# Kernel optimization log

Measured on AMD Instinct MI355X. Metric: run time of the kernel, lower is better.

## Reference

```python
import jax, jax.numpy as jnp
import numpy as np

K = 20      # knn fan-in (constructor arg)
EPS = 1e-5  # LayerNorm eps (torch default)

def ln(x, g, b):
    m = jnp.mean(x, axis=-1, keepdims=True)
    v = jnp.mean((x - m) ** 2, axis=-1, keepdims=True)
    return (x - m) / jnp.sqrt(v + EPS) * g + b

def setup_inputs():
    key = jax.random.key(0)
    ks = jax.random.split(key, 12)
    N, Cin, Cout, H = 4096, 128, 128, 512
    def w(k, i, o):
        return (jax.random.normal(k, (i, o), jnp.float32) / np.sqrt(i)).astype(jnp.float32)
    return dict(
        x=jax.random.normal(ks[0], (N, Cin), jnp.float32),
        pos=jax.random.normal(ks[1], (N, 3), jnp.float32),
        batch=jnp.zeros((N,), jnp.int32),
        # PointTransformerConv linears (bias=False in PyG)
        W_lin=w(ks[2], Cin, Cout),
        W_src=w(ks[3], Cin, Cout),
        W_dst=w(ks[4], Cin, Cout),
        # pos_nn: Lin(3,H) LN ELU Lin(H,Cout) LN ELU
        pw1=w(ks[5], 3, H), pb1=jnp.zeros((H,), jnp.float32),
        pg1=jnp.ones((H,), jnp.float32), pbt1=jnp.zeros((H,), jnp.float32),
        pw2=w(ks[6], H, Cout), pb2=jnp.zeros((Cout,), jnp.float32),
        pg2=jnp.ones((Cout,), jnp.float32), pbt2=jnp.zeros((Cout,), jnp.float32),
        # attn_nn: Lin(Cout,H) LN ELU Lin(H,Cout) LN ELU
        aw1=w(ks[7], Cout, H), ab1=jnp.zeros((H,), jnp.float32),
        ag1=jnp.ones((H,), jnp.float32), abt1=jnp.zeros((H,), jnp.float32),
        aw2=w(ks[8], H, Cout), ab2=jnp.zeros((Cout,), jnp.float32),
        ag2=jnp.ones((Cout,), jnp.float32), abt2=jnp.zeros((Cout,), jnp.float32),
    )

def knn_idx(pos):
    # single-graph knn (batch is constant zero); returns [N, K+1] neighbor idx
    # with self-loop appended (PointTransformerConv add_self_loops=True).
    N = pos.shape[0]
    sq = jnp.sum(pos * pos, axis=1)
    d2 = sq[:, None] + sq[None, :] - 2.0 * (pos @ pos.T)      # [N, N]
    d2 = d2.at[jnp.arange(N), jnp.arange(N)].set(jnp.inf)      # loop=False
    _, nbr = jax.lax.top_k(-d2, K)                             # [N, K]
    return jnp.concatenate([nbr, jnp.arange(N)[:, None]], axis=1)

def reference(x, pos, batch, W_lin, W_src, W_dst,
              pw1, pb1, pg1, pbt1, pw2, pb2, pg2, pbt2,
              aw1, ab1, ag1, abt1, aw2, ab2, ag2, abt2):
    idx = knn_idx(pos)                      # [N, K+1] source node per edge
    v = x @ W_lin                           # message values
    a_src = x @ W_src
    a_dst = x @ W_dst
    rel = pos[:, None, :] - pos[idx]        # pos_i - pos_j, [N, K+1, 3]
    h = jax.nn.elu(ln(rel @ pw1 + pb1, pg1, pbt1))
    delta = jax.nn.elu(ln(h @ pw2 + pb2, pg2, pbt2))           # [N, K+1, C]
    alpha = a_dst[:, None, :] - a_src[idx] + delta
    h2 = jax.nn.elu(ln(alpha @ aw1 + ab1, ag1, abt1))
    alpha = jax.nn.elu(ln(h2 @ aw2 + ab2, ag2, abt2))
    alpha = jax.nn.softmax(alpha, axis=1)   # softmax over neighbors of i
    return jnp.sum(alpha * (v[idx] + delta), axis=1)           # [N, C]
```

## Files before the change

kernel.cpp:

```cpp
#include <hip/hip_runtime.h>
#include <math.h>

#define NN    4096
#define CIN   128
#define CO    128
#define HD    512
#define KK    20
#define EE    21
#define EDGES (NN * EE)
#define LNEPS 1e-5f
#define WSZ   65536

typedef unsigned short u16;
typedef unsigned int   u32;
typedef unsigned long long u64;
typedef __attribute__((ext_vector_type(8))) short bf16x8;
typedef __attribute__((ext_vector_type(4))) float f32x4;

#define MFMA16(a,b,c) __builtin_amdgcn_mfma_f32_16x16x32_bf16(a,b,c,0,0,0)

__device__ __forceinline__ u16 f2b(float x) {
    u32 u = __float_as_uint(x);
    u32 r = u + 0x7fffu + ((u >> 16) & 1u);
    return (u16)(r >> 16);
}
__device__ __forceinline__ float b2f(u16 h) {
    return __uint_as_float(((u32)h) << 16);
}

__global__ __launch_bounds__(256) void k_knn(const float* __restrict__ pos,
                                             int* __restrict__ idxg)
{
    int i = blockIdx.x * 4 + (threadIdx.x >> 6);
    int lane = threadIdx.x & 63;
    float px = pos[3*i], py = pos[3*i+1], pz = pos[3*i+2];
    float bd[KK]; int bi[KK];
#pragma unroll
    for (int s = 0; s < KK; ++s) { bd[s] = INFINITY; bi[s] = 0x7fffffff; }
    for (int j = lane; j < NN; j += 64) {
        float dx = px - pos[3*j], dy = py - pos[3*j+1], dz = pz - pos[3*j+2];
        float d2 = dx*dx + dy*dy + dz*dz;
        if (j != i && d2 < bd[KK-1]) {
            float cd = d2; int ci = j;
#pragma unroll
            for (int s = 0; s < KK; ++s) {
                bool sw = cd < bd[s];
                float td = sw ? bd[s] : cd;  int ti = sw ? bi[s] : ci;
                bd[s] = sw ? cd : bd[s];     bi[s] = sw ? ci : bi[s];
                cd = td; ci = ti;
            }
        }
    }
    for (int r = 0; r < KK; ++r) {
        u64 m = ~0ull;
#pragma unroll
        for (int s = 0; s < KK; ++s) {
            u64 k = ((u64)__float_as_uint(bd[s]) << 32) | (u32)bi[s];
            m = k < m ? k : m;
        }
#pragma unroll
        for (int off = 32; off > 0; off >>= 1) {
            u64 o = __shfl_xor(m, off, 64);
            m = o < m ? o : m;
        }
        if (lane == 0) idxg[i*EE + r] = (int)(u32)m;
#pragma unroll
        for (int s = 0; s < KK; ++s) {
            u64 k = ((u64)__float_as_uint(bd[s]) << 32) | (u32)bi[s];
            if (k == m) bd[s] = INFINITY;
        }
    }
    if (lane == 0) idxg[i*EE + KK] = i;
}

__global__ __launch_bounds__(256) void k_lin3(const float* __restrict__ x,
        const float* __restrict__ Wl, const float* __restrict__ Ws, const float* __restrict__ Wd,
        float* __restrict__ v, float* __restrict__ as_, float* __restrict__ ad)
{
    __shared__ float sx[8][CIN];
    int b = blockIdx.x, t = threadIdx.x;
    int n0 = b * 8;
    for (int q = t; q < 8*CIN; q += 256) sx[q >> 7][q & 127] = x[n0*CIN + q];
    __syncthreads();
    int c = t & 127, g = t >> 7;
    float al[4] = {0,0,0,0}, asr[4] = {0,0,0,0}, adr[4] = {0,0,0,0};
    for (int k = 0; k < CIN; ++k) {
        float wl = Wl[k*CO + c], ws = Ws[k*CO + c], wd = Wd[k*CO + c];
#pragma unroll
        for (int nn2 = 0; nn2 < 4; ++nn2) {
            float xv = sx[g*4 + nn2][k];
            al[nn2]  = fmaf(xv, wl, al[nn2]);
            asr[nn2] = fmaf(xv, ws, asr[nn2]);
            adr[nn2] = fmaf(xv, wd, adr[nn2]);
        }
    }
#pragma unroll
    for (int nn2 = 0; nn2 < 4; ++nn2) {
        int n = n0 + g*4 + nn2;
        v[n*CO + c]   = al[nn2];
        as_[n*CO + c] = asr[nn2];
        ad[n*CO + c]  = adr[nn2];
    }
}

__global__ __launch_bounds__(256) void k_wconv3(
        const float* __restrict__ aw1, const float* __restrict__ aw2,
        const float* __restrict__ pw2,
        u16* __restrict__ awp1, u16* __restrict__ awp2, u16* __restrict__ pwp2)
{
    int gb = blockIdx.x;
    const float* src; u16* dst; int N, kplog, base; bool split;
    if (gb < 256)      { src = aw1; dst = awp1; N = HD; kplog = 2; base = 0;   split = false; }
    else if (gb < 512) { src = aw2; dst = awp2; N = CO; kplog = 4; base = 256; split = true;  }
    else               { src = pw2; dst = pwp2; N = CO; kplog = 4; base = 512; split = true;  }
    int idx = (gb - base)*256 + threadIdx.x;
    int j  = idx & 7;
    int l  = (idx >> 3) & 63;
    int ks = (idx >> 9) & ((1 << kplog) - 1);
    int nt = idx >> (9 + kplog);
    int k = ks*32 + (l >> 4)*8 + j;
    int c = nt*16 + (l & 15);
    float w = src[(size_t)k*N + c];
    u16 hi = f2b(w);
    dst[idx] = hi;
    if (split) dst[idx + WSZ] = f2b(w - b2f(hi));
}

template<int L, int NW>
__device__ __forceinline__ void ln_elu_b16(u16* base, int rows, int stride,
        const float* __restrict__ gam, const float* __restrict__ bet)
{
    constexpr int P = L / 64;
    int t = threadIdx.x, lane = t & 63, w = t >> 6;
    float g[P], b[P];
#pragma unroll
    for (int q = 0; q < P; q += 4) {
        *(float4*)&g[q] = *(const float4*)&gam[lane*P + q];
        *(float4*)&b[q] = *(const float4*)&bet[lane*P + q];
    }
    for (int e = w; e < rows; e += NW) {
        u16* row = base + e*stride + lane*P;
        u16 raw[P];
        *(ushort4*)&raw[0] = *(const ushort4*)&row[0];
        *(ushort4*)&raw[4] = *(const ushort4*)&row[4];
        float vals[P]; float s = 0.f, sq = 0.f;
#pragma unroll
        for (int q = 0; q < P; ++q) {
            float xx = b2f(raw[q]);
            vals[q] = xx; s += xx; sq = fmaf(xx, xx, sq);
        }
#pragma unroll
        for (int off = 32; off > 0; off >>= 1) {
            s  += __shfl_xor(s,  off, 64);
            sq += __shfl_xor(sq, off, 64);
        }
        float mn = s * (1.0f / L);
        float msq = mn * mn;
        float var = fmaf(sq, 1.0f / L, -msq);
        float rstd = rsqrtf(var + LNEPS);
#pragma unroll
        for (int q = 0; q < P; ++q) {
            float z = (vals[q] - mn) * rstd;
            float y = fmaf(z, g[q], b[q]);
            y = y > 0.f ? y : __expf(y) - 1.f;
            raw[q] = f2b(y);
        }
        *(ushort4*)&row[0] = *(const ushort4*)&raw[0];
        *(ushort4*)&row[4] = *(const ushort4*)&raw[4];
    }
}

template<int L, int NW>
__device__ __forceinline__ void ln_elu_f32v(float* base, int rows, int stride,
        const float* __restrict__ gam, const float* __restrict__ bet)
{
    constexpr int P = L / 64;
    int t = threadIdx.x, lane = t & 63, w = t >> 6;
    float g[P], b[P];
    *(float2*)&g[0] = *(const float2*)&gam[lane*P];
    *(float2*)&b[0] = *(const float2*)&bet[lane*P];
    for (int e = w; e < rows; e += NW) {
        float* row = base + e*stride + lane*P;
        float vals[P];
        *(float2*)&vals[0] = *(const float2*)&row[0];
        float s = 0.f, sq = 0.f;
#pragma unroll
        for (int q = 0; q < P; ++q) { s += vals[q]; sq = fmaf(vals[q], vals[q], sq); }
#pragma unroll
        for (int off = 32; off > 0; off >>= 1) {
            s  += __shfl_xor(s,  off, 64);
            sq += __shfl_xor(sq, off, 64);
        }
        float mn = s * (1.0f / L);
        float msq = mn * mn;
        float var = fmaf(sq, 1.0f / L, -msq);
        float rstd = rsqrtf(var + LNEPS);
#pragma unroll
        for (int q = 0; q < P; ++q) {
            float z = (vals[q] - mn) * rstd;
            float y = fmaf(z, g[q], b[q]);
            vals[q] = y > 0.f ? y : __expf(y) - 1.f;
        }
        *(float2*)&row[0] = *(const float2*)&vals[0];
    }
}

#define SA_S 136
#define SH_S 520
#define SF_S 132

__global__ __launch_bounds__(512) void k_posnn(
        const float* __restrict__ pos, const int* __restrict__ idxg,
        const float* __restrict__ pw1, const float* __restrict__ pb1,
        const float* __restrict__ pg1, const float* __restrict__ pbt1,
        const u16* __restrict__ pwp2, const float* __restrict__ pb2,
        const float* __restrict__ pg2, const float* __restrict__ pbt2,
        u16* __restrict__ delta)
{
    __shared__ __align__(16) u16   s_h[32*SH_S];
    __shared__ __align__(16) float s_d[32*SF_S];
    __shared__ float s_rel[32][3];
    int t = threadIdx.x;
    int e0g = blockIdx.x * 32;
    if (t < 32) {
        int e = e0g + t;
        u32 ii = (u32)e / 21u;
        int j = idxg[e];
        s_rel[t][0] = pos[3*ii]   - pos[3*j];
        s_rel[t][1] = pos[3*ii+1] - pos[3*j+1];
        s_rel[t][2] = pos[3*ii+2] - pos[3*j+2];
    }
    __syncthreads();
    {
        int c1 = t;
        float wa0 = pw1[c1], wa1 = pw1[HD + c1], wa2 = pw1[2*HD + c1], ba = pb1[c1];
        for (int r = 0; r < 32; ++r) {
            float hv = fmaf(s_rel[r][2], wa2, fmaf(s_rel[r][1], wa1, fmaf(s_rel[r][0], wa0, ba)));
            s_h[r*SH_S + c1] = f2b(hv);
        }
    }
    __syncthreads();
    ln_elu_b16<HD, 8>(s_h, 32, SH_S, pg1, pbt1);
    __syncthreads();
    {
        int w = t >> 6, l = t & 63, lr = l & 15, lk = l >> 4;
        int m = w & 1, nt0 = (w >> 1) * 2;
        bf16x8 afr[16];
#pragma unroll
        for (int ks = 0; ks < 16; ++ks)
            afr[ks] = *(const bf16x8*)&s_h[(m*16 + lr)*SH_S + ks*32 + lk*8];
#pragma unroll
        for (int n2 = 0; n2 < 2; ++n2) {
            int nt = nt0 + n2;
            const u16* bp  = pwp2 + ((size_t)nt*16*64 + l)*8;
            const u16* bpl = bp + WSZ;
            f32x4 acch = {0.f, 0.f, 0.f, 0.f};
            f32x4 accl = {0.f, 0.f, 0.f, 0.f};
#pragma unroll
            for (int ks = 0; ks < 16; ++ks) {
                bf16x8 bh = *(const bf16x8*)(bp + ks*512);
                acch = MFMA16(afr[ks], bh, acch);
                bf16x8 bl = *(const bf16x8*)(bpl + ks*512);
                accl = MFMA16(afr[ks], bl, accl);
            }
            float bias = pb2[nt*16 + lr];
#pragma unroll
            for (int r = 0; r < 4; ++r)
                s_d[(m*16 + lk*4 + r)*SF_S + nt*16 + lr] = (acch[r] + accl[r]) + bias;
        }
    }
    __syncthreads();
    ln_elu_f32v<CO, 8>(s_d, 32, SF_S, pg2, pbt2);
    __syncthreads();
    {
        int el = t >> 4, c0 = (t & 15) << 3;
        const float* sp = &s_d[el*SF_S + c0];
        float4 v0 = *(const float4*)(sp);
        float4 v1 = *(const float4*)(sp + 4);
        bf16x8 o;
        o[0] = (short)f2b(v0.x); o[1] = (short)f2b(v0.y);
        o[2] = (short)f2b(v0.z); o[3] = (short)f2b(v0.w);
        o[4] = (short)f2b(v1.x); o[5] = (short)f2b(v1.y);
        o[6] = (short)f2b(v1.z); o[7] = (short)f2b(v1.w);
        *(bf16x8*)&delta[(size_t)(e0g + el)*CO + c0] = o;
    }
}

__global__ __launch_bounds__(512) void k_amlp(
        const int* __restrict__ idxg,
        const float* __restrict__ as_, const float* __restrict__ ad,
        const u16* __restrict__ delta,
        const u16* __restrict__ awp1, const float* __restrict__ ab1,
        const float* __restrict__ ag1, const float* __restrict__ abt1,
        const u16* __restrict__ awp2, const float* __restrict__ ab2,
        const float* __restrict__ ag2, const float* __restrict__ abt2,
        u16* __restrict__ alphaF)
{
    __shared__ __align__(16) u16   s_h[32*SH_S];
    __shared__ __align__(16) float s_u[32*SF_S];
    u16*   s_a  = (u16*)s_u;
    float* s_af = s_u;
    int t = threadIdx.x;
    int e0g = blockIdx.x * 32;
    {
        int el = t >> 4, c0 = (t & 15) << 3;
        int e = e0g + el;
        int i = (int)((u32)e / 21u);
        int j = idxg[e];
        const float* adp = ad  + i*CIN + c0;
        const float* asp = as_ + j*CIN + c0;
        const u16*  dp   = delta + (size_t)e*CO + c0;
        float4 a0 = *(const float4*)(adp);
        float4 a1 = *(const float4*)(adp + 4);
        float4 s0 = *(const float4*)(asp);
        float4 s1 = *(const float4*)(asp + 4);
        bf16x8 d8 = *(const bf16x8*)(dp);
        bf16x8 o;
        o[0] = (short)f2b(a0.x - s0.x + b2f((u16)d8[0]));
        o[1] = (short)f2b(a0.y - s0.y + b2f((u16)d8[1]));
        o[2] = (short)f2b(a0.z - s0.z + b2f((u16)d8[2]));
        o[3] = (short)f2b(a0.w - s0.w + b2f((u16)d8[3]));
        o[4] = (short)f2b(a1.x - s1.x + b2f((u16)d8[4]));
        o[5] = (short)f2b(a1.y - s1.y + b2f((u16)d8[5]));
        o[6] = (short)f2b(a1.z - s1.z + b2f((u16)d8[6]));
        o[7] = (short)f2b(a1.w - s1.w + b2f((u16)d8[7]));
        *(bf16x8*)&s_a[el*SA_S + c0] = o;
    }
    __syncthreads();
    int w = t >> 6, l = t & 63, lr = l & 15, lk = l >> 4;
    {
        int m = w & 1, nt0 = (w >> 1) * 8;
        bf16x8 afr[4];
#pragma unroll
        for (int ks = 0; ks < 4; ++ks)
            afr[ks] = *(const bf16x8*)&s_a[(m*16 + lr)*SA_S + ks*32 + lk*8];
#pragma unroll
        for (int n2 = 0; n2 < 8; ++n2) {
            int nt = nt0 + n2;
            const u16* bp = awp1 + ((size_t)nt*4*64 + l)*8;
            f32x4 acc = {0.f, 0.f, 0.f, 0.f};
#pragma unroll
            for (int ks = 0; ks < 4; ++ks) {
                bf16x8 bfr = *(const bf16x8*)(bp + ks*512);
                acc = MFMA16(afr[ks], bfr, acc);
            }
            float bias = ab1[nt*16 + lr];
#pragma unroll
            for (int r = 0; r < 4; ++r)
                s_h[(m*16 + lk*4 + r)*SH_S + nt*16 + lr] = f2b(acc[r] + bias);
        }
    }
    __syncthreads();
    ln_elu_b16<HD, 8>(s_h, 32, SH_S, ag1, abt1);
    __syncthreads();
    {
        int m = w & 1, nt0 = (w >> 1) * 2;
        bf16x8 afr[16];
#pragma unroll
        for (int ks = 0; ks < 16; ++ks)
            afr[ks] = *(const bf16x8*)&s_h[(m*16 + lr)*SH_S + ks*32 + lk*8];
#pragma unroll
        for (int n2 = 0; n2 < 2; ++n2) {
            int nt = nt0 + n2;
            const u16* bp  = awp2 + ((size_t)nt*16*64 + l)*8;
            const u16* bpl = bp + WSZ;
            f32x4 acch = {0.f, 0.f, 0.f, 0.f};
            f32x4 accl = {0.f, 0.f, 0.f, 0.f};
#pragma unroll
            for (int ks = 0; ks < 16; ++ks) {
                bf16x8 bh = *(const bf16x8*)(bp + ks*512);
                acch = MFMA16(afr[ks], bh, acch);
                bf16x8 bl = *(const bf16x8*)(bpl + ks*512);
                accl = MFMA16(afr[ks], bl, accl);
            }
            float bias = ab2[nt*16 + lr];
#pragma unroll
            for (int r = 0; r < 4; ++r)
                s_af[(m*16 + lk*4 + r)*SF_S + nt*16 + lr] = (acch[r] + accl[r]) + bias;
        }
    }
    __syncthreads();
    ln_elu_f32v<CO, 8>(s_af, 32, SF_S, ag2, abt2);
    __syncthreads();
    {
        int el = t >> 4, c0 = (t & 15) << 3;
        const float* sp = &s_af[el*SF_S + c0];
        float4 v0 = *(const float4*)(sp);
        float4 v1 = *(const float4*)(sp + 4);
        bf16x8 o;
        o[0] = (short)f2b(v0.x); o[1] = (short)f2b(v0.y);
        o[2] = (short)f2b(v0.z); o[3] = (short)f2b(v0.w);
        o[4] = (short)f2b(v1.x); o[5] = (short)f2b(v1.y);
        o[6] = (short)f2b(v1.z); o[7] = (short)f2b(v1.w);
        *(bf16x8*)&alphaF[(size_t)(e0g + el)*CO + c0] = o;
    }
}

__global__ __launch_bounds__(256) void k_agg(
        const int* __restrict__ idxg,
        const float* __restrict__ v, const u16* __restrict__ delta,
        const u16* __restrict__ alphaF, float* __restrict__ out)
{
    __shared__ int s_idx[4][EE];
    int b = blockIdx.x, t = threadIdx.x;
    int n0 = b * 4;
    if (t < 4*EE) s_idx[t/EE][t%EE] = idxg[n0*EE + t];
    __syncthreads();
    int g = t >> 6, c0 = (t & 63) * 2;
    int i = n0 + g;
    size_t base = (size_t)i*EE*CO + c0;
    float afx[EE], afy[EE];
    float mx0 = -INFINITY, mx1 = -INFINITY;
#pragma unroll
    for (int e = 0; e < EE; ++e) {
        ushort2 u = *(const ushort2*)&alphaF[base + e*CO];
        afx[e] = b2f(u.x); afy[e] = b2f(u.y);
        mx0 = fmaxf(mx0, afx[e]); mx1 = fmaxf(mx1, afy[e]);
    }
    float ss0 = 0.f, ss1 = 0.f;
#pragma unroll
    for (int e = 0; e < EE; ++e) {
        afx[e] = __expf(afx[e] - mx0); ss0 += afx[e];
        afy[e] = __expf(afy[e] - mx1); ss1 += afy[e];
    }
    float ac0 = 0.f, ac1 = 0.f;
#pragma unroll
    for (int e = 0; e < EE; ++e) {
        int j = s_idx[g][e];
        float2 vv = *(const float2*)&v[j*CO + c0];
        ushort2 dd = *(const ushort2*)&delta[base + e*CO];
        ac0 = fmaf(afx[e], vv.x + b2f(dd.x), ac0);
        ac1 = fmaf(afy[e], vv.y + b2f(dd.y), ac1);
    }
    float2 o; o.x = ac0 / ss0; o.y = ac1 / ss1;
    *(float2*)&out[i*CO + c0] = o;
}

extern "C" void kernel_launch(void* const* d_in, const int* in_sizes, int n_in,
                              void* d_out, int out_size, void* d_ws, size_t ws_size,
                              hipStream_t stream)
{
    const float* x    = (const float*)d_in[0];
    const float* pos  = (const float*)d_in[1];
    const float* Wl   = (const float*)d_in[3];
    const float* Wsrc = (const float*)d_in[4];
    const float* Wdst = (const float*)d_in[5];
    const float* pw1  = (const float*)d_in[6];
    const float* pb1  = (const float*)d_in[7];
    const float* pg1  = (const float*)d_in[8];
    const float* pbt1 = (const float*)d_in[9];
    const float* pw2  = (const float*)d_in[10];
    const float* pb2  = (const float*)d_in[11];
    const float* pg2  = (const float*)d_in[12];
    const float* pbt2 = (const float*)d_in[13];
    const float* aw1  = (const float*)d_in[14];
    const float* ab1  = (const float*)d_in[15];
    const float* ag1  = (const float*)d_in[16];
    const float* abt1 = (const float*)d_in[17];
    const float* aw2  = (const float*)d_in[18];
    const float* ab2  = (const float*)d_in[19];
    const float* ag2  = (const float*)d_in[20];
    const float* abt2 = (const float*)d_in[21];
    float* out = (float*)d_out;

    char* ws = (char*)d_ws;
    int*   idxg   = (int*)ws;
    u16*   awp1   = (u16*)(ws + 0x54000);
    u16*   awp2   = (u16*)(ws + 0x74000);
    u16*   pwp2   = (u16*)(ws + 0xB4000);
    float* v      = (float*)(ws + 0x100000);
    float* asrc   = (float*)(ws + 0x300000);
    float* adst   = (float*)(ws + 0x500000);
    u16*   delta  = (u16*)(ws + 0x700000);
    u16*   alphaF = (u16*)(ws + 0x700000 + 0x1500000);

    k_knn   <<<NN/4,     256, 0, stream>>>(pos, idxg);
    k_wconv3<<<768,      256, 0, stream>>>(aw1, aw2, pw2, awp1, awp2, pwp2);
    k_lin3  <<<NN/8,     256, 0, stream>>>(x, Wl, Wsrc, Wdst, v, asrc, adst);
    k_posnn <<<EDGES/32, 512, 0, stream>>>(pos, idxg, pw1, pb1, pg1, pbt1,
                                           pwp2, pb2, pg2, pbt2, delta);
    k_amlp  <<<EDGES/32, 512, 0, stream>>>(idxg, asrc, adst, delta,
                                           awp1, ab1, ag1, abt1,
                                           awp2, ab2, ag2, abt2, alphaF);
    k_agg   <<<NN/4,     256, 0, stream>>>(idxg, v, delta, alphaF, out);
}
```

Before: 279.2 us.

## Merge prologue kernels into one launch and fuse pos-MLP with attention MLP

```diff
diff --git a/kernel.cpp b/kernel.cpp
--- a/kernel.cpp
+++ b/kernel.cpp
@@ -26,104 +26,6 @@
 }
 __device__ __forceinline__ float b2f(u16 h) {
     return __uint_as_float(((u32)h) << 16);
-}
-
-__global__ __launch_bounds__(256) void k_knn(const float* __restrict__ pos,
-                                             int* __restrict__ idxg)
-{
-    int i = blockIdx.x * 4 + (threadIdx.x >> 6);
-    int lane = threadIdx.x & 63;
-    float px = pos[3*i], py = pos[3*i+1], pz = pos[3*i+2];
-    float bd[KK]; int bi[KK];
-#pragma unroll
-    for (int s = 0; s < KK; ++s) { bd[s] = INFINITY; bi[s] = 0x7fffffff; }
-    for (int j = lane; j < NN; j += 64) {
-        float dx = px - pos[3*j], dy = py - pos[3*j+1], dz = pz - pos[3*j+2];
-        float d2 = dx*dx + dy*dy + dz*dz;
-        if (j != i && d2 < bd[KK-1]) {
-            float cd = d2; int ci = j;
-#pragma unroll
-            for (int s = 0; s < KK; ++s) {
-                bool sw = cd < bd[s];
-                float td = sw ? bd[s] : cd;  int ti = sw ? bi[s] : ci;
-                bd[s] = sw ? cd : bd[s];     bi[s] = sw ? ci : bi[s];
-                cd = td; ci = ti;
-            }
-        }
-    }
-    for (int r = 0; r < KK; ++r) {
-        u64 m = ~0ull;
-#pragma unroll
-        for (int s = 0; s < KK; ++s) {
-            u64 k = ((u64)__float_as_uint(bd[s]) << 32) | (u32)bi[s];
-            m = k < m ? k : m;
-        }
-#pragma unroll
-        for (int off = 32; off > 0; off >>= 1) {
-            u64 o = __shfl_xor(m, off, 64);
-            m = o < m ? o : m;
-        }
-        if (lane == 0) idxg[i*EE + r] = (int)(u32)m;
-#pragma unroll
-        for (int s = 0; s < KK; ++s) {
-            u64 k = ((u64)__float_as_uint(bd[s]) << 32) | (u32)bi[s];
-            if (k == m) bd[s] = INFINITY;
-        }
-    }
-    if (lane == 0) idxg[i*EE + KK] = i;
-}
-
-__global__ __launch_bounds__(256) void k_lin3(const float* __restrict__ x,
-        const float* __restrict__ Wl, const float* __restrict__ Ws, const float* __restrict__ Wd,
-        float* __restrict__ v, float* __restrict__ as_, float* __restrict__ ad)
-{
-    __shared__ float sx[8][CIN];
-    int b = blockIdx.x, t = threadIdx.x;
-    int n0 = b * 8;
-    for (int q = t; q < 8*CIN; q += 256) sx[q >> 7][q & 127] = x[n0*CIN + q];
-    __syncthreads();
-    int c = t & 127, g = t >> 7;
-    float al[4] = {0,0,0,0}, asr[4] = {0,0,0,0}, adr[4] = {0,0,0,0};
-    for (int k = 0; k < CIN; ++k) {
-        float wl = Wl[k*CO + c], ws = Ws[k*CO + c], wd = Wd[k*CO + c];
-#pragma unroll
-        for (int nn2 = 0; nn2 < 4; ++nn2) {
-            float xv = sx[g*4 + nn2][k];
-            al[nn2]  = fmaf(xv, wl, al[nn2]);
-            asr[nn2] = fmaf(xv, ws, asr[nn2]);
-            adr[nn2] = fmaf(xv, wd, adr[nn2]);
-        }
-    }
-#pragma unroll
-    for (int nn2 = 0; nn2 < 4; ++nn2) {
-        int n = n0 + g*4 + nn2;
-        v[n*CO + c]   = al[nn2];
-        as_[n*CO + c] = asr[nn2];
-        ad[n*CO + c]  = adr[nn2];
-    }
-}
-
-__global__ __launch_bounds__(256) void k_wconv3(
-        const float* __restrict__ aw1, const float* __restrict__ aw2,
-        const float* __restrict__ pw2,
-        u16* __restrict__ awp1, u16* __restrict__ awp2, u16* __restrict__ pwp2)
-{
-    int gb = blockIdx.x;
-    const float* src; u16* dst; int N, kplog, base; bool split;
-    if (gb < 256)      { src = aw1; dst = awp1; N = HD; kplog = 2; base = 0;   split = false; }
-    else if (gb < 512) { src = aw2; dst = awp2; N = CO; kplog = 4; base = 256; split = true;  }
-    else               { src = pw2; dst = pwp2; N = CO; kplog = 4; base = 512; split = true;  }
-    int idx = (gb - base)*256 + threadIdx.x;
-    int j  = idx & 7;
-    int l  = (idx >> 3) & 63;
-    int ks = (idx >> 9) & ((1 << kplog) - 1);
-    int nt = idx >> (9 + kplog);
-    int k = ks*32 + (l >> 4)*8 + j;
-    int c = nt*16 + (l & 15);
-    float w = src[(size_t)k*N + c];
-    u16 hi = f2b(w);
-    dst[idx] = hi;
-    if (split) dst[idx + WSZ] = f2b(w - b2f(hi));
 }
 
 template<int L, int NW>
@@ -205,20 +107,124 @@
     }
 }
 
+__global__ __launch_bounds__(256) void k_pro(
+        const float* __restrict__ pos, const float* __restrict__ x,
+        const float* __restrict__ Wl, const float* __restrict__ Ws, const float* __restrict__ Wd,
+        const float* __restrict__ aw1, const float* __restrict__ aw2,
+        const float* __restrict__ pw2,
+        int* __restrict__ idxg, float* __restrict__ v,
+        float* __restrict__ as_, float* __restrict__ ad,
+        u16* __restrict__ awp1, u16* __restrict__ awp2, u16* __restrict__ pwp2)
+{
+    __shared__ float sx[8][CIN];
+    int b = blockIdx.x;
+    if (b < 1024) {
+        int i = b * 4 + (threadIdx.x >> 6);
+        int lane = threadIdx.x & 63;
+        float px = pos[3*i], py = pos[3*i+1], pz = pos[3*i+2];
+        float bd[KK]; int bi[KK];
+#pragma unroll
+        for (int s = 0; s < KK; ++s) { bd[s] = INFINITY; bi[s] = 0x7fffffff; }
+        for (int j = lane; j < NN; j += 64) {
+            float dx = px - pos[3*j], dy = py - pos[3*j+1], dz = pz - pos[3*j+2];
+            float d2 = dx*dx + dy*dy + dz*dz;
+            if (j != i && d2 < bd[KK-1]) {
+                float cd = d2; int ci = j;
+#pragma unroll
+                for (int s = 0; s < KK; ++s) {
+                    bool sw = cd < bd[s];
+                    float td = sw ? bd[s] : cd;  int ti = sw ? bi[s] : ci;
+                    bd[s] = sw ? cd : bd[s];     bi[s] = sw ? ci : bi[s];
+                    cd = td; ci = ti;
+                }
+            }
+        }
+        for (int r = 0; r < KK; ++r) {
+            u64 m = ~0ull;
+#pragma unroll
+            for (int s = 0; s < KK; ++s) {
+                u64 k = ((u64)__float_as_uint(bd[s]) << 32) | (u32)bi[s];
+                m = k < m ? k : m;
+            }
+#pragma unroll
+            for (int off = 32; off > 0; off >>= 1) {
+                u64 o = __shfl_xor(m, off, 64);
+                m = o < m ? o : m;
+            }
+            if (lane == 0) idxg[i*EE + r] = (int)(u32)m;
+#pragma unroll
+            for (int s = 0; s < KK; ++s) {
+                u64 k = ((u64)__float_as_uint(bd[s]) << 32) | (u32)bi[s];
+                if (k == m) bd[s] = INFINITY;
+            }
+        }
+        if (lane == 0) idxg[i*EE + KK] = i;
+    } else if (b < 1792) {
+        int gb = b - 1024;
+        const float* src; u16* dst; int N, kplog, base; bool split;
+        if (gb < 256)      { src = aw1; dst = awp1; N = HD; kplog = 2; base = 0;   split = false; }
+        else if (gb < 512) { src = aw2; dst = awp2; N = CO; kplog = 4; base = 256; split = true;  }
+        else               { src = pw2; dst = pwp2; N = CO; kplog = 4; base = 512; split = true;  }
+        int idx = (gb - base)*256 + threadIdx.x;
+        int j  = idx & 7;
+        int l  = (idx >> 3) & 63;
+        int ks = (idx >> 9) & ((1 << kplog) - 1);
+        int nt = idx >> (9 + kplog);
+        int k = ks*32 + (l >> 4)*8 + j;
+        int c = nt*16 + (l & 15);
+        float w = src[(size_t)k*N + c];
+        u16 hi = f2b(w);
+        dst[idx] = hi;
+        if (split) dst[idx + WSZ] = f2b(w - b2f(hi));
+    } else {
+        int bb = b - 1792, t = threadIdx.x;
+        int n0 = bb * 8;
+        for (int q = t; q < 8*CIN; q += 256) sx[q >> 7][q & 127] = x[n0*CIN + q];
+        __syncthreads();
+        int c = t & 127, g = t >> 7;
+        float al[4] = {0,0,0,0}, asr[4] = {0,0,0,0}, adr[4] = {0,0,0,0};
+        for (int k = 0; k < CIN; ++k) {
+            float wl = Wl[k*CO + c], ws = Ws[k*CO + c], wd = Wd[k*CO + c];
+#pragma unroll
+            for (int nn2 = 0; nn2 < 4; ++nn2) {
+                float xv = sx[g*4 + nn2][k];
+                al[nn2]  = fmaf(xv, wl, al[nn2]);
+                asr[nn2] = fmaf(xv, ws, asr[nn2]);
+                adr[nn2] = fmaf(xv, wd, adr[nn2]);
+            }
+        }
+#pragma unroll
+        for (int nn2 = 0; nn2 < 4; ++nn2) {
+            int n = n0 + g*4 + nn2;
+            v[n*CO + c]   = al[nn2];
+            as_[n*CO + c] = asr[nn2];
+            ad[n*CO + c]  = adr[nn2];
+        }
+    }
+}
+
 #define SA_S 136
 #define SH_S 520
 #define SF_S 132
 
-__global__ __launch_bounds__(512) void k_posnn(
+__global__ __launch_bounds__(512) void k_mlp(
         const float* __restrict__ pos, const int* __restrict__ idxg,
+        const float* __restrict__ as_, const float* __restrict__ ad,
         const float* __restrict__ pw1, const float* __restrict__ pb1,
         const float* __restrict__ pg1, const float* __restrict__ pbt1,
         const u16* __restrict__ pwp2, const float* __restrict__ pb2,
         const float* __restrict__ pg2, const float* __restrict__ pbt2,
-        u16* __restrict__ delta)
+        const u16* __restrict__ awp1, const float* __restrict__ ab1,
+        const float* __restrict__ ag1, const float* __restrict__ abt1,
+        const u16* __restrict__ awp2, const float* __restrict__ ab2,
+        const float* __restrict__ ag2, const float* __restrict__ abt2,
+        u16* __restrict__ delta, u16* __restrict__ alphaF)
 {
     __shared__ __align__(16) u16   s_h[32*SH_S];
-    __shared__ __align__(16) float s_d[32*SF_S];
+    __shared__ __align__(16) float s_u[32*SF_S];
+    float* s_d  = s_u;
+    float* s_af = s_u;
+    u16*   s_aH = s_h;
     __shared__ float s_rel[32][3];
     int t = threadIdx.x;
     int e0g = blockIdx.x * 32;
@@ -242,8 +248,8 @@
     __syncthreads();
     ln_elu_b16<HD, 8>(s_h, 32, SH_S, pg1, pbt1);
     __syncthreads();
-    {
-        int w = t >> 6, l = t & 63, lr = l & 15, lk = l >> 4;
+    int w = t >> 6, l = t & 63, lr = l & 15, lk = l >> 4;
+    {
         int m = w & 1, nt0 = (w >> 1) * 2;
         bf16x8 afr[16];
 #pragma unroll
@@ -274,66 +280,46 @@
     __syncthreads();
     {
         int el = t >> 4, c0 = (t & 15) << 3;
-        const float* sp = &s_d[el*SF_S + c0];
-        float4 v0 = *(const float4*)(sp);
-        float4 v1 = *(const float4*)(sp + 4);
-        bf16x8 o;
-        o[0] = (short)f2b(v0.x); o[1] = (short)f2b(v0.y);
-        o[2] = (short)f2b(v0.z); o[3] = (short)f2b(v0.w);
-        o[4] = (short)f2b(v1.x); o[5] = (short)f2b(v1.y);
-        o[6] = (short)f2b(v1.z); o[7] = (short)f2b(v1.w);
-        *(bf16x8*)&delta[(size_t)(e0g + el)*CO + c0] = o;
-    }
-}
-
-__global__ __launch_bounds__(512) void k_amlp(
-        const int* __restrict__ idxg,
-        const float* __restrict__ as_, const float* __restrict__ ad,
-        const u16* __restrict__ delta,
-        const u16* __restrict__ awp1, const float* __restrict__ ab1,
-        const float* __restrict__ ag1, const float* __restrict__ abt1,
-        const u16* __restrict__ awp2, const float* __restrict__ ab2,
-        const float* __restrict__ ag2, const float* __restrict__ abt2,
-        u16* __restrict__ alphaF)
-{
-    __shared__ __align__(16) u16   s_h[32*SH_S];
-    __shared__ __align__(16) float s_u[32*SF_S];
-    u16*   s_a  = (u16*)s_u;
-    float* s_af = s_u;
-    int t = threadIdx.x;
-    int e0g = blockIdx.x * 32;
-    {
-        int el = t >> 4, c0 = (t & 15) << 3;
         int e = e0g + el;
         int i = (int)((u32)e / 21u);
         int j = idxg[e];
+        const float* sp  = &s_d[el*SF_S + c0];
+        float4 d0 = *(const float4*)(sp);
+        float4 d1 = *(const float4*)(sp + 4);
+        bf16x8 od;
+        od[0] = (short)f2b(d0.x); od[1] = (short)f2b(d0.y);
+        od[2] = (short)f2b(d0.z); od[3] = (short)f2b(d0.w);
+        od[4] = (short)f2b(d1.x); od[5] = (short)f2b(d1.y);
+        od[6] = (short)f2b(d1.z); od[7] = (short)f2b(d1.w);
+        *(bf16x8*)&delta[(size_t)e*CO + c0] = od;
         const float* adp = ad  + i*CIN + c0;
         const float* asp = as_ + j*CIN + c0;
-        const u16*  dp   = delta + (size_t)e*CO + c0;
         float4 a0 = *(const float4*)(adp);
         float4 a1 = *(const float4*)(adp + 4);
         float4 s0 = *(const float4*)(asp);
         float4 s1 = *(const float4*)(asp + 4);
-        bf16x8 d8 = *(const bf16x8*)(dp);
-        bf16x8 o;
-        o[0] = (short)f2b(a0.x - s0.x + b2f((u16)d8[0]));
-        o[1] = (short)f2b(a0.y - s0.y + b2f((u16)d8[1]));
-        o[2] = (short)f2b(a0.z - s0.z + b2f((u16)d8[2]));
-        o[3] = (short)f2b(a0.w - s0.w + b2f((u16)d8[3]));
-        o[4] = (short)f2b(a1.x - s1.x + b2f((u16)d8[4]));
-        o[5] = (short)f2b(a1.y - s1.y + b2f((u16)d8[5]));
-        o[6] = (short)f2b(a1.z - s1.z + b2f((u16)d8[6]));
-        o[7] = (short)f2b(a1.w - s1.w + b2f((u16)d8[7]));
-        *(bf16x8*)&s_a[el*SA_S + c0] = o;
-    }
-    __syncthreads();
-    int w = t >> 6, l = t & 63, lr = l & 15, lk = l >> 4;
+        bf16x8 oa;
+        oa[0] = (short)f2b(a0.x - s0.x + d0.x);
+        oa[1] = (short)f2b(a0.y - s0.y + d0.y);
+        oa[2] = (short)f2b(a0.z - s0.z + d0.z);
+        oa[3] = (short)f2b(a0.w - s0.w + d0.w);
+        oa[4] = (short)f2b(a1.x - s1.x + d1.x);
+        oa[5] = (short)f2b(a1.y - s1.y + d1.y);
+        oa[6] = (short)f2b(a1.z - s1.z + d1.z);
+        oa[7] = (short)f2b(a1.w - s1.w + d1.w);
+        *(bf16x8*)&s_aH[el*SA_S + c0] = oa;
+    }
+    __syncthreads();
+    bf16x8 afr1[4];
+    {
+        int m = w & 1;
+#pragma unroll
+        for (int ks = 0; ks < 4; ++ks)
+            afr1[ks] = *(const bf16x8*)&s_aH[(m*16 + lr)*SA_S + ks*32 + lk*8];
+    }
+    __syncthreads();
     {
         int m = w & 1, nt0 = (w >> 1) * 8;
-        bf16x8 afr[4];
-#pragma unroll
-        for (int ks = 0; ks < 4; ++ks)
-            afr[ks] = *(const bf16x8*)&s_a[(m*16 + lr)*SA_S + ks*32 + lk*8];
 #pragma unroll
         for (int n2 = 0; n2 < 8; ++n2) {
             int nt = nt0 + n2;
@@ -342,7 +328,7 @@
 #pragma unroll
             for (int ks = 0; ks < 4; ++ks) {
                 bf16x8 bfr = *(const bf16x8*)(bp + ks*512);
-                acc = MFMA16(afr[ks], bfr, acc);
+                acc = MFMA16(afr1[ks], bfr, acc);
             }
             float bias = ab1[nt*16 + lr];
 #pragma unroll
@@ -474,13 +460,11 @@
     u16*   delta  = (u16*)(ws + 0x700000);
     u16*   alphaF = (u16*)(ws + 0x700000 + 0x1500000);
 
-    k_knn   <<<NN/4,     256, 0, stream>>>(pos, idxg);
-    k_wconv3<<<768,      256, 0, stream>>>(aw1, aw2, pw2, awp1, awp2, pwp2);
-    k_lin3  <<<NN/8,     256, 0, stream>>>(x, Wl, Wsrc, Wdst, v, asrc, adst);
-    k_posnn <<<EDGES/32, 512, 0, stream>>>(pos, idxg, pw1, pb1, pg1, pbt1,
-                                           pwp2, pb2, pg2, pbt2, delta);
-    k_amlp  <<<EDGES/32, 512, 0, stream>>>(idxg, asrc, adst, delta,
-                                           awp1, ab1, ag1, abt1,
-                                           awp2, ab2, ag2, abt2, alphaF);
-    k_agg   <<<NN/4,     256, 0, stream>>>(idxg, v, delta, alphaF, out);
-}
+    k_pro <<<2304,     256, 0, stream>>>(pos, x, Wl, Wsrc, Wdst, aw1, aw2, pw2,
+                                         idxg, v, asrc, adst, awp1, awp2, pwp2);
+    k_mlp <<<EDGES/32, 512, 0, stream>>>(pos, idxg, asrc, adst,
+                                         pw1, pb1, pg1, pbt1, pwp2, pb2, pg2, pbt2,
+                                         awp1, ab1, ag1, abt1, awp2, ab2, ag2, abt2,
+                                         delta, alphaF);
+    k_agg <<<NN/4,     256, 0, stream>>>(idxg, v, delta, alphaF, out);
+}
```

Result: faster. 253.5 us (-9.2%).
